# Performance work log

Hardware: AMD Instinct MI355X
Metric: run time of the kernel (lower is better)

The kernel has to match this reference:

```python
import jax, jax.numpy as jnp
import numpy as np

NUM_HEADS = 32
NUM_KV_HEADS = 8
HEAD_DIM = 128
ROPE_THETA = 10000.0
MAX_SEQ_LEN = 2048


def build_rope_cache(seq_len, head_dim, theta=10000.0):
    freq_indices = jnp.arange(0, head_dim, 2, dtype=jnp.float32)
    inv_freq = 1.0 / theta ** (freq_indices / head_dim)
    positions = jnp.arange(seq_len, dtype=jnp.float32)
    angles = jnp.outer(positions, inv_freq)  # (S, D/2)
    cos = jnp.cos(angles)
    sin = jnp.sin(angles)
    return jnp.concatenate([cos, cos], axis=-1), jnp.concatenate([sin, sin], axis=-1)


def apply_rotary_embedding(x, cos, sin):
    # x: (B, S, H, D); cos/sin: (S, D)
    d = x.shape[-1]
    x1, x2 = x[..., : d // 2], x[..., d // 2 :]
    x_rot = jnp.concatenate([-x2, x1], axis=-1)
    return x * cos[None, :, None, :] + x_rot * sin[None, :, None, :]


def setup_inputs() -> dict:
    key = jax.random.key(0)
    k_x, k_q, k_k, k_v, k_o = jax.random.split(key, 5)
    B, S, HID = 2, 2048, NUM_HEADS * HEAD_DIM
    KV = NUM_KV_HEADS * HEAD_DIM
    x = jax.random.normal(k_x, (B, S, HID), dtype=jnp.float32)
    # causal mask, shape (B, 1, S, S)
    causal = jnp.tril(jnp.ones((S, S), dtype=bool))
    mask = jnp.broadcast_to(causal[None, None], (B, 1, S, S))
    sc_in = 1.0 / np.sqrt(HID)
    Wq = jax.random.normal(k_q, (HID, HID), dtype=jnp.float32) * sc_in
    Wk = jax.random.normal(k_k, (HID, KV), dtype=jnp.float32) * sc_in
    Wv = jax.random.normal(k_v, (HID, KV), dtype=jnp.float32) * sc_in
    Wo = jax.random.normal(k_o, (HID, HID), dtype=jnp.float32) * sc_in
    return {"x": x, "mask": mask, "Wq": Wq, "Wk": Wk, "Wv": Wv, "Wo": Wo}


def reference(x, mask, Wq, Wk, Wv, Wo):
    B, S, _ = x.shape
    q = (x @ Wq).reshape(B, S, NUM_HEADS, HEAD_DIM)
    k = (x @ Wk).reshape(B, S, NUM_KV_HEADS, HEAD_DIM)
    v = (x @ Wv).reshape(B, S, NUM_KV_HEADS, HEAD_DIM)
    cos, sin = build_rope_cache(MAX_SEQ_LEN, HEAD_DIM, ROPE_THETA)
    cos, sin = cos[:S], sin[:S]
    q = apply_rotary_embedding(q, cos, sin)
    k = apply_rotary_embedding(k, cos, sin)
    group = NUM_HEADS // NUM_KV_HEADS
    if group > 1:
        k = jnp.repeat(k, group, axis=2)
        v = jnp.repeat(v, group, axis=2)
    scale = HEAD_DIM ** -0.5
    # (B, H, S, S)
    scores = jnp.einsum("bqhd,bkhd->bhqk", q, k) * scale
    scores = jnp.where(mask, scores, jnp.finfo(jnp.float32).min)
    attn = jax.nn.softmax(scores, axis=-1)
    out = jnp.einsum("bhqk,bkhd->bqhd", attn, v).reshape(B, S, NUM_HEADS * HEAD_DIM)
    return out @ Wo
```

## Files before the change

### kernel.cpp

```cpp
#include <hip/hip_runtime.h>

#define S_LEN   2048
#define HID_DIM 4096
#define NHEADS  32
#define NKVH    8
#define HD      128
#define KV_DIM  1024
#define KV2     2048
#define BS_ROWS 4096

typedef __attribute__((ext_vector_type(4))) float f32x4;
typedef __attribute__((ext_vector_type(8))) short bf16x8;

__device__ __forceinline__ unsigned short f2b(float f) {
  union { float f; unsigned int u; } cv; cv.f = f;
  unsigned int r = (cv.u + 0x7FFFu + ((cv.u >> 16) & 1u)) >> 16;
  return (unsigned short)r;
}
__device__ __forceinline__ float b2f(unsigned short u) {
  union { unsigned int u; float f; } cv; cv.u = ((unsigned int)u) << 16; return cv.f;
}
__device__ __forceinline__ void gload_lds16(const void* g, void* l) {
  __builtin_amdgcn_global_load_lds(
      (const __attribute__((address_space(1))) unsigned int*)g,
      (__attribute__((address_space(3))) unsigned int*)l, 16, 0, 0);
}
__device__ __forceinline__ float exp2fast(float x) {
#if __has_builtin(__builtin_amdgcn_exp2f)
  return __builtin_amdgcn_exp2f(x);
#else
  return exp2f(x);
#endif
}
__device__ __forceinline__ unsigned cvtpk(float a, float b) {
  unsigned r;
  asm("v_cvt_pk_bf16_f32 %0, %1, %2" : "=v"(r) : "v"(a), "v"(b));
  return r;
}
__device__ __forceinline__ void store_out(float* p, float v) { *p = v; }
__device__ __forceinline__ void store_out(unsigned short* p, float v) { *p = f2b(v); }

__global__ void cvt_f32_bf16(const float* __restrict__ in, unsigned short* __restrict__ out, int n4) {
  int i = blockIdx.x * blockDim.x + threadIdx.x;
  if (i >= n4) return;
  f32x4 v = reinterpret_cast<const f32x4*>(in)[i];
  ushort4 o;
  o.x = f2b(v[0]); o.y = f2b(v[1]); o.z = f2b(v[2]); o.w = f2b(v[3]);
  reinterpret_cast<ushort4*>(out)[i] = o;
}

__global__ void transpose_cvt(const float* __restrict__ W, unsigned short* __restrict__ Wt,
                              int K, int N) {
  __shared__ float t[32][33];
  int n0 = blockIdx.x * 32, k0 = blockIdx.y * 32;
  int tx = threadIdx.x, ty = threadIdx.y;
#pragma unroll
  for (int i = 0; i < 4; ++i)
    t[ty + 8 * i][tx] = W[(size_t)(k0 + ty + 8 * i) * N + n0 + tx];
  __syncthreads();
#pragma unroll
  for (int i = 0; i < 4; ++i)
    Wt[(size_t)(n0 + ty + 8 * i) * K + k0 + tx] = f2b(t[tx][ty + 8 * i]);
}

__global__ void transpose_v_k(const unsigned short* __restrict__ KVb, unsigned short* __restrict__ Vt) {
  __shared__ unsigned short t[32][33];
  int c0 = blockIdx.x * 32;
  int r0 = blockIdx.y * 32;
  int tx = threadIdx.x, ty = threadIdx.y;
#pragma unroll
  for (int i = 0; i < 4; ++i)
    t[ty + 8 * i][tx] = KVb[(size_t)(r0 + ty + 8 * i) * KV2 + KV_DIM + c0 + tx];
  __syncthreads();
  int ob = (r0 >> 11) * 1024;
  int oc = r0 & 2047;
#pragma unroll
  for (int i = 0; i < 4; ++i)
    Vt[(size_t)(ob + c0 + ty + 8 * i) * S_LEN + oc + tx] = t[tx][ty + 8 * i];
}

__global__ void rope_table_k(float* __restrict__ cosT, float* __restrict__ sinT) {
  int idx = blockIdx.x * blockDim.x + threadIdx.x;
  if (idx >= S_LEN * 64) return;
  int s = idx >> 6, i = idx & 63;
  float inv = 1.0f / powf(10000.0f, (float)(2 * i) * (1.0f / 128.0f));
  float ang = (float)s * inv;
  cosT[idx] = cosf(ang);
  sinT[idx] = sinf(ang);
}

__global__ void rope_apply_k(unsigned short* __restrict__ X, const float* __restrict__ cosT,
                             const float* __restrict__ sinT, int nheads, int rowstride,
                             float scale, int total) {
  int idx = blockIdx.x * blockDim.x + threadIdx.x;
  if (idx >= total) return;
  int i4 = idx & 15;
  int t = idx >> 4;
  int h = t % nheads;
  int row = t / nheads;
  int s = row & (S_LEN - 1);
  f32x4 c4 = *reinterpret_cast<const f32x4*>(&cosT[(s << 6) + i4 * 4]);
  f32x4 s4 = *reinterpret_cast<const f32x4*>(&sinT[(s << 6) + i4 * 4]);
  size_t base = (size_t)row * rowstride + (size_t)h * HD + i4 * 4;
  ushort4 xa = *reinterpret_cast<const ushort4*>(&X[base]);
  ushort4 xb = *reinterpret_cast<const ushort4*>(&X[base + 64]);
  unsigned short* pa = (unsigned short*)&xa;
  unsigned short* pb = (unsigned short*)&xb;
  ushort4 oa, ob;
  unsigned short* qa = (unsigned short*)&oa;
  unsigned short* qb = (unsigned short*)&ob;
#pragma unroll
  for (int j = 0; j < 4; ++j) {
    float x1 = b2f(pa[j]), x2 = b2f(pb[j]);
    qa[j] = f2b((x1 * c4[j] - x2 * s4[j]) * scale);
    qb[j] = f2b((x2 * c4[j] + x1 * s4[j]) * scale);
  }
  *reinterpret_cast<ushort4*>(&X[base])      = oa;
  *reinterpret_cast<ushort4*>(&X[base + 64]) = ob;
}

template <typename OutT>
__global__ __launch_bounds__(256) void gemm_bt(const unsigned short* __restrict__ A,
                                               const unsigned short* __restrict__ Bt,
                                               OutT* __restrict__ C, int M, int N, int K) {
  __shared__ unsigned short As[128 * 32];
  __shared__ unsigned short Bs[128 * 32];
  const int tid = threadIdx.x;
  const int lane = tid & 63;
  const int wave = tid >> 6;
  int nwg = gridDim.x, wg = blockIdx.x;
  int swz = (nwg % 8 == 0) ? ((wg & 7) * (nwg >> 3) + (wg >> 3)) : wg;
  const int nbn = N >> 7;
  const int bm = swz / nbn, bn = swz % nbn;
  const int m0 = bm << 7, n0 = bn << 7;
  const int wr = wave >> 1, wc = wave & 1;
  const int lr = lane & 15, kb = lane >> 4;

  f32x4 acc[4][4];
#pragma unroll
  for (int i = 0; i < 4; ++i)
#pragma unroll
    for (int j = 0; j < 4; ++j) acc[i][j] = (f32x4){0.f, 0.f, 0.f, 0.f};

  const unsigned short* Ab = A + (size_t)m0 * K;
  const unsigned short* Bb = Bt + (size_t)n0 * K;

  for (int k0 = 0; k0 < K; k0 += 32) {
    __syncthreads();
#pragma unroll
    for (int i = 0; i < 2; ++i) {
      int idx = i * 256 + tid;
      int row = idx >> 2;
      int off = (idx & 3) << 3;
      gload_lds16(Ab + (size_t)row * K + k0 + off, As + row * 32 + off);
      gload_lds16(Bb + (size_t)row * K + k0 + off, Bs + row * 32 + off);
    }
    __syncthreads();

    bf16x8 af[4], bfr[4];
#pragma unroll
    for (int mi = 0; mi < 4; ++mi)
      af[mi] = *reinterpret_cast<const bf16x8*>(As + (wr * 64 + mi * 16 + lr) * 32 + kb * 8);
#pragma unroll
    for (int ni = 0; ni < 4; ++ni)
      bfr[ni] = *reinterpret_cast<const bf16x8*>(Bs + (wc * 64 + ni * 16 + lr) * 32 + kb * 8);
#pragma unroll
    for (int mi = 0; mi < 4; ++mi)
#pragma unroll
      for (int ni = 0; ni < 4; ++ni)
        acc[mi][ni] = __builtin_amdgcn_mfma_f32_16x16x32_bf16(af[mi], bfr[ni], acc[mi][ni], 0, 0, 0);
  }

#pragma unroll
  for (int mi = 0; mi < 4; ++mi)
#pragma unroll
    for (int ni = 0; ni < 4; ++ni)
#pragma unroll
      for (int r = 0; r < 4; ++r) {
        int row = m0 + wr * 64 + mi * 16 + kb * 4 + r;
        int col = n0 + wc * 64 + ni * 16 + lr;
        store_out(&C[(size_t)row * N + col], acc[mi][ni][r]);
      }
}

#define STAGE_HALF(dstBase, Sp, k0, h)                                           \
  {                                                                              \
    _Pragma("unroll")                                                            \
    for (int i_ = 0; i_ < 2; ++i_) {                                             \
      int c_ = i_ * 512 + tid;                                                   \
      int rl_ = c_ >> 3, ch_ = c_ & 7;                                           \
      int row_ = (h) * 128 + rl_;                                                \
      gload_lds16((Sp) + (size_t)row_ * K + (k0) + ((ch_ ^ (row_ & 7)) << 3),    \
                  (char*)(dstBase) + row_ * 128 + ch_ * 16);                     \
    }                                                                            \
  }
#define LDF(buf, R, sw) \
  (*reinterpret_cast<const bf16x8*>((const char*)(buf) + (R) * 128 + (sw)))
#define PHASE_SYNC()                                        \
  __builtin_amdgcn_s_barrier();                             \
  asm volatile("s_waitcnt lgkmcnt(0)" ::: "memory");        \
  __builtin_amdgcn_sched_barrier(0);

template <typename OutT>
__global__ __launch_bounds__(512, 1) void gemm256(const unsigned short* __restrict__ A,
                                                  const unsigned short* __restrict__ Bt,
                                                  OutT* __restrict__ C, int M, int N, int K) {
  __shared__ unsigned short Asl[2][256 * 64];
  __shared__ unsigned short Bsl[2][256 * 64];
  const int tid = threadIdx.x;
  const int lane = tid & 63;
  const int wave = tid >> 6;
  const int wr = wave >> 2;
  const int wc = wave & 3;
  const int lr = lane & 15, kb = lane >> 4;

// ... 71 lines not shown
      for (int ni = 0; ni < 4; ++ni)
        acc[mi][ni] = __builtin_amdgcn_mfma_f32_16x16x32_bf16(af[mi], bfr[ni], acc[mi][ni], 0, 0, 0);
    __builtin_amdgcn_s_setprio(0);
    __builtin_amdgcn_s_barrier();

#pragma unroll
    for (int mi = 0; mi < 4; ++mi) af[mi] = LDF(Acur, wr * 128 + (mi + 4) * 16 + lr, sw1);
    PHASE_SYNC();
    __builtin_amdgcn_s_setprio(1);
#pragma unroll
    for (int mi = 0; mi < 4; ++mi)
#pragma unroll
      for (int ni = 0; ni < 4; ++ni)
        acc[mi + 4][ni] = __builtin_amdgcn_mfma_f32_16x16x32_bf16(af[mi], bfr[ni], acc[mi + 4][ni], 0, 0, 0);
    __builtin_amdgcn_s_setprio(0);
    __builtin_amdgcn_s_barrier();

    if (pf) asm volatile("s_waitcnt vmcnt(0)" ::: "memory");
    __builtin_amdgcn_s_barrier();
  }

#pragma unroll
  for (int mi = 0; mi < 8; ++mi)
#pragma unroll
    for (int ni = 0; ni < 4; ++ni)
#pragma unroll
      for (int r = 0; r < 4; ++r) {
        int row = m0 + wr * 128 + mi * 16 + kb * 4 + r;
        int col = n0 + wc * 64 + ni * 16 + lr;
        store_out(&C[(size_t)row * N + col], acc[mi][ni][r]);
      }
}

__global__ __launch_bounds__(256, 2) void attn_fwd(const unsigned short* __restrict__ Q,
                                                   const unsigned short* __restrict__ KV,
                                                   const unsigned short* __restrict__ Vt,
                                                   const float* __restrict__ cosT,
                                                   const float* __restrict__ sinT,
                                                   unsigned short* __restrict__ O) {
  __shared__ unsigned short Ks[2][64 * 128];
  __shared__ unsigned short Ps[4][2][16 * 72];
  const int tid = threadIdx.x, lane = tid & 63, wave = tid >> 6;
  const int lr = lane & 15, kb = lane >> 4;
  const int pr = blockIdx.x;
  const int bh = blockIdx.y;
  const int b = bh >> 5, h = bh & 31, kvh = h >> 2;
  const unsigned short* Qp = Q + (size_t)b * S_LEN * HID_DIM + (size_t)h * HD;
  const unsigned short* Kp = KV + (size_t)b * S_LEN * KV2 + (size_t)kvh * HD;
  const unsigned short* Vtp = Vt + (size_t)(b * 8 + kvh) * HD * S_LEN;
  unsigned short* Op = O + (size_t)b * S_LEN * HID_DIM + (size_t)h * HD;

#pragma unroll 1
  for (int pass = 0; pass < 2; ++pass) {
    const int qt = pass ? pr : 15 - pr;
    const int q0 = qt * 128;
    int qrowQ[2];
    qrowQ[0] = q0 + wave * 32 + lr;
    qrowQ[1] = q0 + wave * 32 + 16 + lr;

    bf16x8 qf[2][4];
#pragma unroll
    for (int qs = 0; qs < 2; ++qs) {
      const int qrow = qrowQ[qs];
      bf16x8 raw[4];
#pragma unroll
      for (int dc = 0; dc < 4; ++dc)
        raw[dc] = *reinterpret_cast<const bf16x8*>(Qp + (size_t)qrow * HID_DIM + dc * 32 + kb * 8);
      const float* ct = cosT + (qrow << 6) + kb * 8;
      const float* st = sinT + (qrow << 6) + kb * 8;
      f32x4 cv0 = *(const f32x4*)(ct),      cv1 = *(const f32x4*)(ct + 4);
      f32x4 cv2 = *(const f32x4*)(ct + 32), cv3 = *(const f32x4*)(ct + 36);
      f32x4 sv0 = *(const f32x4*)(st),      sv1 = *(const f32x4*)(st + 4);
      f32x4 sv2 = *(const f32x4*)(st + 32), sv3 = *(const f32x4*)(st + 36);
      const float sc = 0.08838834764831843f * 1.4426950408889634f;
#pragma unroll
      for (int j = 0; j < 8; ++j) {
        const int jj = j & 3;
        float c0 = (j < 4) ? cv0[jj] : cv1[jj];
        float s0 = (j < 4) ? sv0[jj] : sv1[jj];
        float c1 = (j < 4) ? cv2[jj] : cv3[jj];
        float s1 = (j < 4) ? sv2[jj] : sv3[jj];
        float a1 = b2f((unsigned short)raw[0][j]), a2 = b2f((unsigned short)raw[2][j]);
        qf[qs][0][j] = (short)f2b((a1 * c0 - a2 * s0) * sc);
        qf[qs][2][j] = (short)f2b((a2 * c0 + a1 * s0) * sc);
        float b1 = b2f((unsigned short)raw[1][j]), b2x = b2f((unsigned short)raw[3][j]);
        qf[qs][1][j] = (short)f2b((b1 * c1 - b2x * s1) * sc);
        qf[qs][3][j] = (short)f2b((b2x * c1 + b1 * s1) * sc);
      }
    }

    f32x4 of[2][8];
#pragma unroll
    for (int qs = 0; qs < 2; ++qs)
#pragma unroll
      for (int i = 0; i < 8; ++i) of[qs][i] = (f32x4){0.f, 0.f, 0.f, 0.f};
    float mrow[2] = {-3.0e38f, -3.0e38f};
    float lrow[2] = {0.f, 0.f};

    const int nsteps = 2 * qt + 2;

#pragma unroll
    for (int i = 0; i < 4; ++i) {
      int c = i * 256 + tid;
      int key = c >> 4;
      int ch = (c & 15) ^ (key & 7);
      gload_lds16(Kp + (size_t)key * KV2 + ch * 8, &Ks[0][0] + c * 8);
    }
    __syncthreads();

#pragma unroll 1
    for (int t = 0; t < nsteps; ++t) {
      const int kv0 = t << 6;
      const unsigned short* Kcur = &Ks[t & 1][0];

      bf16x8 vf[8];
#pragma unroll
      for (int dc2 = 0; dc2 < 8; ++dc2)
        vf[dc2] = *reinterpret_cast<const bf16x8*>(
            Vtp + (size_t)(dc2 * 16 + lr) * S_LEN + kv0 + kb * 8);

      if (t + 1 < nsteps) {
        unsigned short* Knxt = &Ks[(t + 1) & 1][0];
#pragma unroll
        for (int i = 0; i < 4; ++i) {
          int c = i * 256 + tid;
          int key = c >> 4;
          int ch = (c & 15) ^ (key & 7);
          gload_lds16(Kp + (size_t)(kv0 + 64 + key) * KV2 + ch * 8, Knxt + c * 8);
        }
      }

      f32x4 sf[2][4];
#pragma unroll
      for (int qs = 0; qs < 2; ++qs)
#pragma unroll
        for (int ki = 0; ki < 4; ++ki) sf[qs][ki] = (f32x4){0.f, 0.f, 0.f, 0.f};
#pragma unroll
      for (int ki = 0; ki < 4; ++ki)
#pragma unroll
        for (int dc = 0; dc < 4; ++dc) {
          bf16x8 kf = *reinterpret_cast<const bf16x8*>(
              Kcur + (ki * 16 + lr) * 128 + (((dc * 4 + kb) ^ (lr & 7)) << 3));
          sf[0][ki] = __builtin_amdgcn_mfma_f32_16x16x32_bf16(kf, qf[0][dc], sf[0][ki], 0, 0, 0);
          sf[1][ki] = __builtin_amdgcn_mfma_f32_16x16x32_bf16(kf, qf[1][dc], sf[1][ki], 0, 0, 0);
        }

#pragma unroll
      for (int qs = 0; qs < 2; ++qs) {
        if (kv0 + 63 > q0 + wave * 32 + qs * 16) {
          const int thr = qrowQ[qs] - kv0;
#pragma unroll
          for (int ki = 0; ki < 4; ++ki)
#pragma unroll
            for (int r = 0; r < 4; ++r)
              if (ki * 16 + kb * 4 + r > thr) sf[qs][ki][r] = -3.0e38f;
        }
      }

#pragma unroll
      for (int qs = 0; qs < 2; ++qs) {
        float m8 = -3.0e38f;
#pragma unroll
        for (int ki = 0; ki < 4; ++ki)
#pragma unroll
          for (int r = 0; r < 4; ++r) m8 = fmaxf(m8, sf[qs][ki][r]);
        m8 = fmaxf(m8, __shfl_xor(m8, 16));
        m8 = fmaxf(m8, __shfl_xor(m8, 32));
        if (__any(m8 > mrow[qs] + 11.5f)) {
          float mn = fmaxf(mrow[qs], m8);
          float corr = exp2fast(mrow[qs] - mn);
          lrow[qs] *= corr;
#pragma unroll
          for (int r = 0; r < 4; ++r) {
            float cr = __shfl(corr, kb * 4 + r);
#pragma unroll
            for (int dc2 = 0; dc2 < 8; ++dc2) of[qs][dc2][r] *= cr;
          }
          mrow[qs] = mn;
        }
        float rs = 0.f;
#pragma unroll
        for (int ki = 0; ki < 4; ++ki) {
          float p0 = exp2fast(sf[qs][ki][0] - mrow[qs]);
          float p1 = exp2fast(sf[qs][ki][1] - mrow[qs]);
          float p2 = exp2fast(sf[qs][ki][2] - mrow[qs]);
          float p3 = exp2fast(sf[qs][ki][3] - mrow[qs]);
          rs += (p0 + p1) + (p2 + p3);
          uint2 w;
          w.x = cvtpk(p0, p1);
          w.y = cvtpk(p2, p3);
          *reinterpret_cast<uint2*>(&Ps[wave][qs][lr * 72 + ki * 16 + kb * 4]) = w;
        }
        rs += __shfl_xor(rs, 16);
        rs += __shfl_xor(rs, 32);
        lrow[qs] += rs;
      }
      asm volatile("s_waitcnt lgkmcnt(0)" ::: "memory");
      __builtin_amdgcn_sched_barrier(0);

      {
        bf16x8 pf0 = *reinterpret_cast<const bf16x8*>(&Ps[wave][0][lr * 72 + kb * 8]);
        bf16x8 pf1 = *reinterpret_cast<const bf16x8*>(&Ps[wave][1][lr * 72 + kb * 8]);
#pragma unroll
        for (int dc2 = 0; dc2 < 8; ++dc2) {
          of[0][dc2] = __builtin_amdgcn_mfma_f32_16x16x32_bf16(pf0, vf[dc2], of[0][dc2], 0, 0, 0);
          of[1][dc2] = __builtin_amdgcn_mfma_f32_16x16x32_bf16(pf1, vf[dc2], of[1][dc2], 0, 0, 0);
        }
      }
#pragma unroll
      for (int dc2 = 0; dc2 < 8; ++dc2)
        vf[dc2] = *reinterpret_cast<const bf16x8*>(
            Vtp + (size_t)(dc2 * 16 + lr) * S_LEN + kv0 + 32 + kb * 8);
      {
        bf16x8 pf0 = *reinterpret_cast<const bf16x8*>(&Ps[wave][0][lr * 72 + 32 + kb * 8]);
        bf16x8 pf1 = *reinterpret_cast<const bf16x8*>(&Ps[wave][1][lr * 72 + 32 + kb * 8]);
#pragma unroll
        for (int dc2 = 0; dc2 < 8; ++dc2) {
          of[0][dc2] = __builtin_amdgcn_mfma_f32_16x16x32_bf16(pf0, vf[dc2], of[0][dc2], 0, 0, 0);
          of[1][dc2] = __builtin_amdgcn_mfma_f32_16x16x32_bf16(pf1, vf[dc2], of[1][dc2], 0, 0, 0);
        }
      }

      __syncthreads();
    }

#pragma unroll
    for (int qs = 0; qs < 2; ++qs) {
      float linv[4];
#pragma unroll
      for (int r = 0; r < 4; ++r) linv[r] = 1.0f / __shfl(lrow[qs], kb * 4 + r);
#pragma unroll
      for (int dc2 = 0; dc2 < 8; ++dc2)
#pragma unroll
        for (int r = 0; r < 4; ++r) {
          int qg = q0 + wave * 32 + qs * 16 + kb * 4 + r;
          Op[(size_t)qg * HID_DIM + dc2 * 16 + lr] = f2b(of[qs][dc2][r] * linv[r]);
        }
    }
  }
}

extern "C" void kernel_launch(void* const* d_in, const int* in_sizes, int n_in,
                              void* d_out, int out_size, void* d_ws, size_t ws_size,
                              hipStream_t stream) {
  const float* x  = (const float*)d_in[0];
  const float* Wq = (const float*)d_in[2];
  const float* Wk = (const float*)d_in[3];
  const float* Wv = (const float*)d_in[4];
  const float* Wo = (const float*)d_in[5];
  float* out = (float*)d_out;

  char* ws = (char*)d_ws;
  unsigned short* xb  = (unsigned short*)(ws + 0);
  unsigned short* wtb = (unsigned short*)(ws + 33554432);
  unsigned short* wkt = (unsigned short*)(ws + 67108864);
  unsigned short* wvt = (unsigned short*)(ws + 75497472);
  unsigned short* Qb  = (unsigned short*)(ws + 83886080);
  unsigned short* KVb = (unsigned short*)(ws + 117440512);
  float* cosT = (float*)(ws + 134217728);
  float* sinT = (float*)(ws + 134742016);
  unsigned short* AO  = xb;
  unsigned short* Vtb = wkt;

  cvt_f32_bf16<<<16384, 256, 0, stream>>>(x, xb, (BS_ROWS * HID_DIM) / 4);
  transpose_cvt<<<dim3(128, 128), dim3(32, 8), 0, stream>>>(Wq, wtb, HID_DIM, HID_DIM);
  transpose_cvt<<<dim3(32, 128), dim3(32, 8), 0, stream>>>(Wk, wkt, HID_DIM, KV_DIM);
  transpose_cvt<<<dim3(32, 128), dim3(32, 8), 0, stream>>>(Wv, wvt, HID_DIM, KV_DIM);
  rope_table_k<<<512, 256, 0, stream>>>(cosT, sinT);

  gemm256<unsigned short><<<256, 512, 0, stream>>>(xb, wtb, Qb, BS_ROWS, HID_DIM, HID_DIM);
  gemm_bt<unsigned short><<<512, 256, 0, stream>>>(xb, wkt, KVb, BS_ROWS, KV2, HID_DIM);

  transpose_v_k<<<dim3(32, 128), dim3(32, 8), 0, stream>>>(KVb, Vtb);
  transpose_cvt<<<dim3(128, 128), dim3(32, 8), 0, stream>>>(Wo, wtb, HID_DIM, HID_DIM);

  rope_apply_k<<<2048, 256, 0, stream>>>(KVb, cosT, sinT, NKVH, KV2, 1.0f,
                                         BS_ROWS * NKVH * 16);

  attn_fwd<<<dim3(8, 64), 256, 0, stream>>>(Qb, KVb, Vtb, cosT, sinT, AO);

  gemm256<float><<<256, 512, 0, stream>>>(AO, wtb, out, BS_ROWS, HID_DIM, HID_DIM);
}
```

Before: 559.0 us.

## Merge prep/post-KV kernels and skip fully-masked attention tiles per wave

Fuses the x conversion, Wq/Wk/Wv transposes and rope table into one prep launch, and fuses K rope with the V transpose into one launch, cutting launch count and inter-kernel gaps. In attention, each wave now skips the QK, softmax and PV work and the V loads for KV tiles lying wholly beyond its causal rows. Both V halves are loaded up front, and the softmax/PV for the two query subtiles is interleaved. This raises register pressure from the extra V fragments, and the waves in a block now do uneven amounts of work.

```diff
diff --git a/kernel.cpp b/kernel.cpp
--- a/kernel.cpp
+++ b/kernel.cpp
@@ -40,13 +40,57 @@
 __device__ __forceinline__ void store_out(float* p, float v) { *p = v; }
 __device__ __forceinline__ void store_out(unsigned short* p, float v) { *p = f2b(v); }
 
-__global__ void cvt_f32_bf16(const float* __restrict__ in, unsigned short* __restrict__ out, int n4) {
-  int i = blockIdx.x * blockDim.x + threadIdx.x;
-  if (i >= n4) return;
-  f32x4 v = reinterpret_cast<const f32x4*>(in)[i];
-  ushort4 o;
-  o.x = f2b(v[0]); o.y = f2b(v[1]); o.z = f2b(v[2]); o.w = f2b(v[3]);
-  reinterpret_cast<ushort4*>(out)[i] = o;
+__global__ __launch_bounds__(256) void prep_k(const float* __restrict__ x,
+                                              unsigned short* __restrict__ xb,
+                                              const float* __restrict__ Wq,
+                                              unsigned short* __restrict__ wtb,
+                                              const float* __restrict__ Wk,
+                                              unsigned short* __restrict__ wkt,
+                                              const float* __restrict__ Wv,
+                                              unsigned short* __restrict__ wvt,
+                                              float* __restrict__ cosT,
+                                              float* __restrict__ sinT) {
+  __shared__ float t[32][33];
+  int bid = blockIdx.x;
+  const int tid = threadIdx.x;
+  if (bid < 16384) {
+    int i = bid * 256 + tid;
+    f32x4 v = reinterpret_cast<const f32x4*>(x)[i];
+    ushort4 o;
+    o.x = f2b(v[0]); o.y = f2b(v[1]); o.z = f2b(v[2]); o.w = f2b(v[3]);
+    reinterpret_cast<ushort4*>(xb)[i] = o;
+    return;
+  }
+  bid -= 16384;
+  const float* W; unsigned short* Wt; int Kd, Nd, bx, by;
+  if (bid < 16384) { W = Wq; Wt = wtb; Kd = HID_DIM; Nd = HID_DIM; bx = bid & 127; by = bid >> 7; }
+  else {
+    bid -= 16384;
+    if (bid < 4096) { W = Wk; Wt = wkt; Kd = HID_DIM; Nd = KV_DIM; bx = bid & 31; by = bid >> 5; }
+    else {
+      bid -= 4096;
+      if (bid < 4096) { W = Wv; Wt = wvt; Kd = HID_DIM; Nd = KV_DIM; bx = bid & 31; by = bid >> 5; }
+      else {
+        bid -= 4096;
+        int idx = bid * 256 + tid;
+        int s = idx >> 6, i = idx & 63;
+        float inv = 1.0f / powf(10000.0f, (float)(2 * i) * (1.0f / 128.0f));
+        float ang = (float)s * inv;
+        cosT[idx] = cosf(ang);
+        sinT[idx] = sinf(ang);
+        return;
+      }
+    }
+  }
+  const int tx = tid & 31, ty = tid >> 5;
+  const int n0 = bx * 32, k0 = by * 32;
+#pragma unroll
+  for (int i = 0; i < 4; ++i)
+    t[ty + 8 * i][tx] = W[(size_t)(k0 + ty + 8 * i) * Nd + n0 + tx];
+  __syncthreads();
+#pragma unroll
+  for (int i = 0; i < 4; ++i)
+    Wt[(size_t)(n0 + ty + 8 * i) * Kd + k0 + tx] = f2b(t[tx][ty + 8 * i]);
 }
 
 __global__ void transpose_cvt(const float* __restrict__ W, unsigned short* __restrict__ Wt,
@@ -63,60 +107,53 @@
     Wt[(size_t)(n0 + ty + 8 * i) * K + k0 + tx] = f2b(t[tx][ty + 8 * i]);
 }
 
-__global__ void transpose_v_k(const unsigned short* __restrict__ KVb, unsigned short* __restrict__ Vt) {
-  __shared__ unsigned short t[32][33];
-  int c0 = blockIdx.x * 32;
-  int r0 = blockIdx.y * 32;
-  int tx = threadIdx.x, ty = threadIdx.y;
+__global__ __launch_bounds__(256) void postkv_k(unsigned short* __restrict__ KVb,
+                                                unsigned short* __restrict__ Vt,
+                                                const float* __restrict__ cosT,
+                                                const float* __restrict__ sinT) {
+  __shared__ unsigned short tsh[32][33];
+  int bid = blockIdx.x;
+  const int tid = threadIdx.x;
+  if (bid < 2048) {
+    int idx = bid * 256 + tid;
+    int i4 = idx & 15;
+    int t = idx >> 4;
+    int h = t & (NKVH - 1);
+    int row = t >> 3;
+    int s = row & (S_LEN - 1);
+    f32x4 c4 = *reinterpret_cast<const f32x4*>(&cosT[(s << 6) + i4 * 4]);
+    f32x4 s4 = *reinterpret_cast<const f32x4*>(&sinT[(s << 6) + i4 * 4]);
+    size_t base = (size_t)row * KV2 + (size_t)h * HD + i4 * 4;
+    ushort4 xa = *reinterpret_cast<const ushort4*>(&KVb[base]);
+    ushort4 xb2 = *reinterpret_cast<const ushort4*>(&KVb[base + 64]);
+    unsigned short* pa = (unsigned short*)&xa;
+    unsigned short* pb = (unsigned short*)&xb2;
+    ushort4 oa, ob;
+    unsigned short* qa = (unsigned short*)&oa;
+    unsigned short* qb = (unsigned short*)&ob;
+#pragma unroll
+    for (int j = 0; j < 4; ++j) {
+      float x1 = b2f(pa[j]), x2 = b2f(pb[j]);
+      qa[j] = f2b(x1 * c4[j] - x2 * s4[j]);
+      qb[j] = f2b(x2 * c4[j] + x1 * s4[j]);
+    }
+    *reinterpret_cast<ushort4*>(&KVb[base])      = oa;
+    *reinterpret_cast<ushort4*>(&KVb[base + 64]) = ob;
+    return;
+  }
+  bid -= 2048;
+  const int tx = tid & 31, ty = tid >> 5;
+  int c0 = (bid & 31) * 32;
+  int r0 = (bid >> 5) * 32;
 #pragma unroll
   for (int i = 0; i < 4; ++i)
-    t[ty + 8 * i][tx] = KVb[(size_t)(r0 + ty + 8 * i) * KV2 + KV_DIM + c0 + tx];
+    tsh[ty + 8 * i][tx] = KVb[(size_t)(r0 + ty + 8 * i) * KV2 + KV_DIM + c0 + tx];
   __syncthreads();
-  int ob = (r0 >> 11) * 1024;
+  int ob2 = (r0 >> 11) * 1024;
   int oc = r0 & 2047;
 #pragma unroll
   for (int i = 0; i < 4; ++i)
-    Vt[(size_t)(ob + c0 + ty + 8 * i) * S_LEN + oc + tx] = t[tx][ty + 8 * i];
-}
-
-__global__ void rope_table_k(float* __restrict__ cosT, float* __restrict__ sinT) {
-  int idx = blockIdx.x * blockDim.x + threadIdx.x;
-  if (idx >= S_LEN * 64) return;
-  int s = idx >> 6, i = idx & 63;
-  float inv = 1.0f / powf(10000.0f, (float)(2 * i) * (1.0f / 128.0f));
-  float ang = (float)s * inv;
-  cosT[idx] = cosf(ang);
-  sinT[idx] = sinf(ang);
-}
-
-__global__ void rope_apply_k(unsigned short* __restrict__ X, const float* __restrict__ cosT,
-                             const float* __restrict__ sinT, int nheads, int rowstride,
-                             float scale, int total) {
-  int idx = blockIdx.x * blockDim.x + threadIdx.x;
-  if (idx >= total) return;
-  int i4 = idx & 15;
-  int t = idx >> 4;
-  int h = t % nheads;
-  int row = t / nheads;
-  int s = row & (S_LEN - 1);
-  f32x4 c4 = *reinterpret_cast<const f32x4*>(&cosT[(s << 6) + i4 * 4]);
-  f32x4 s4 = *reinterpret_cast<const f32x4*>(&sinT[(s << 6) + i4 * 4]);
-  size_t base = (size_t)row * rowstride + (size_t)h * HD + i4 * 4;
-  ushort4 xa = *reinterpret_cast<const ushort4*>(&X[base]);
-  ushort4 xb = *reinterpret_cast<const ushort4*>(&X[base + 64]);
-  unsigned short* pa = (unsigned short*)&xa;
-  unsigned short* pb = (unsigned short*)&xb;
-  ushort4 oa, ob;
-  unsigned short* qa = (unsigned short*)&oa;
-  unsigned short* qb = (unsigned short*)&ob;
-#pragma unroll
-  for (int j = 0; j < 4; ++j) {
-    float x1 = b2f(pa[j]), x2 = b2f(pb[j]);
-    qa[j] = f2b((x1 * c4[j] - x2 * s4[j]) * scale);
-    qb[j] = f2b((x2 * c4[j] + x1 * s4[j]) * scale);
-  }
-  *reinterpret_cast<ushort4*>(&X[base])      = oa;
-  *reinterpret_cast<ushort4*>(&X[base + 64]) = ob;
+    Vt[(size_t)(ob2 + c0 + ty + 8 * i) * S_LEN + oc + tx] = tsh[tx][ty + 8 * i];
 }
 
 template <typename OutT>
@@ -398,12 +435,17 @@
     for (int t = 0; t < nsteps; ++t) {
       const int kv0 = t << 6;
       const unsigned short* Kcur = &Ks[t & 1][0];
-
-      bf16x8 vf[8];
-#pragma unroll
-      for (int dc2 = 0; dc2 < 8; ++dc2)
-        vf[dc2] = *reinterpret_cast<const bf16x8*>(
-            Vtp + (size_t)(dc2 * 16 + lr) * S_LEN + kv0 + kb * 8);
+      const bool active = (kv0 <= q0 + wave * 32 + 31);
+
+      bf16x8 vf0[8], vf1[8];
+      if (active) {
+#pragma unroll
+        for (int dc2 = 0; dc2 < 8; ++dc2) {
+          const unsigned short* vr = Vtp + (size_t)(dc2 * 16 + lr) * S_LEN + kv0 + kb * 8;
+          vf0[dc2] = *reinterpret_cast<const bf16x8*>(vr);
+          vf1[dc2] = *reinterpret_cast<const bf16x8*>(vr + 32);
+        }
+      }
 
       if (t + 1 < nsteps) {
         unsigned short* Knxt = &Ks[(t + 1) & 1][0];
@@ -416,94 +458,134 @@
         }
       }
 
-      f32x4 sf[2][4];
-#pragma unroll
-      for (int qs = 0; qs < 2; ++qs)
-#pragma unroll
-        for (int ki = 0; ki < 4; ++ki) sf[qs][ki] = (f32x4){0.f, 0.f, 0.f, 0.f};
-#pragma unroll
-      for (int ki = 0; ki < 4; ++ki)
-#pragma unroll
-        for (int dc = 0; dc < 4; ++dc) {
-          bf16x8 kf = *reinterpret_cast<const bf16x8*>(
-              Kcur + (ki * 16 + lr) * 128 + (((dc * 4 + kb) ^ (lr & 7)) << 3));
-          sf[0][ki] = __builtin_amdgcn_mfma_f32_16x16x32_bf16(kf, qf[0][dc], sf[0][ki], 0, 0, 0);
-          sf[1][ki] = __builtin_amdgcn_mfma_f32_16x16x32_bf16(kf, qf[1][dc], sf[1][ki], 0, 0, 0);
-        }
-
-#pragma unroll
-      for (int qs = 0; qs < 2; ++qs) {
-        if (kv0 + 63 > q0 + wave * 32 + qs * 16) {
-          const int thr = qrowQ[qs] - kv0;
+      if (active) {
+        f32x4 sf[2][4];
+#pragma unroll
+        for (int qs = 0; qs < 2; ++qs)
+#pragma unroll
+          for (int ki = 0; ki < 4; ++ki) sf[qs][ki] = (f32x4){0.f, 0.f, 0.f, 0.f};
+#pragma unroll
+        for (int ki = 0; ki < 4; ++ki)
+#pragma unroll
+          for (int dc = 0; dc < 4; ++dc) {
+            bf16x8 kf = *reinterpret_cast<const bf16x8*>(
+                Kcur + (ki * 16 + lr) * 128 + (((dc * 4 + kb) ^ (lr & 7)) << 3));
+            sf[0][ki] = __builtin_amdgcn_mfma_f32_16x16x32_bf16(kf, qf[0][dc], sf[0][ki], 0, 0, 0);
+            sf[1][ki] = __builtin_amdgcn_mfma_f32_16x16x32_bf16(kf, qf[1][dc], sf[1][ki], 0, 0, 0);
+          }
+
+#pragma unroll
+        for (int qs = 0; qs < 2; ++qs) {
+          if (kv0 + 63 > q0 + wave * 32 + qs * 16) {
+            const int thr = qrowQ[qs] - kv0;
+#pragma unroll
+            for (int ki = 0; ki < 4; ++ki)
+#pragma unroll
+              for (int r = 0; r < 4; ++r)
+                if (ki * 16 + kb * 4 + r > thr) sf[qs][ki][r] = -3.0e38f;
+          }
+        }
+
+        {
+          const int qs = 0;
+          float m8 = -3.0e38f;
 #pragma unroll
           for (int ki = 0; ki < 4; ++ki)
 #pragma unroll
-            for (int r = 0; r < 4; ++r)
-              if (ki * 16 + kb * 4 + r > thr) sf[qs][ki][r] = -3.0e38f;
-        }
-      }
-
-#pragma unroll
-      for (int qs = 0; qs < 2; ++qs) {
-        float m8 = -3.0e38f;
-#pragma unroll
-        for (int ki = 0; ki < 4; ++ki)
-#pragma unroll
-          for (int r = 0; r < 4; ++r) m8 = fmaxf(m8, sf[qs][ki][r]);
-        m8 = fmaxf(m8, __shfl_xor(m8, 16));
-        m8 = fmaxf(m8, __shfl_xor(m8, 32));
-        if (__any(m8 > mrow[qs] + 11.5f)) {
-          float mn = fmaxf(mrow[qs], m8);
-          float corr = exp2fast(mrow[qs] - mn);
-          lrow[qs] *= corr;
-#pragma unroll
-          for (int r = 0; r < 4; ++r) {
-            float cr = __shfl(corr, kb * 4 + r);
-#pragma unroll
-            for (int dc2 = 0; dc2 < 8; ++dc2) of[qs][dc2][r] *= cr;
-          }
-          mrow[qs] = mn;
-        }
-        float rs = 0.f;
-#pragma unroll
-        for (int ki = 0; ki < 4; ++ki) {
-          float p0 = exp2fast(sf[qs][ki][0] - mrow[qs]);
-          float p1 = exp2fast(sf[qs][ki][1] - mrow[qs]);
-          float p2 = exp2fast(sf[qs][ki][2] - mrow[qs]);
-          float p3 = exp2fast(sf[qs][ki][3] - mrow[qs]);
-          rs += (p0 + p1) + (p2 + p3);
-          uint2 w;
-          w.x = cvtpk(p0, p1);
-          w.y = cvtpk(p2, p3);
-          *reinterpret_cast<uint2*>(&Ps[wave][qs][lr * 72 + ki * 16 + kb * 4]) = w;
-        }
-        rs += __shfl_xor(rs, 16);
-        rs += __shfl_xor(rs, 32);
-        lrow[qs] += rs;
-      }
-      asm volatile("s_waitcnt lgkmcnt(0)" ::: "memory");
-      __builtin_amdgcn_sched_barrier(0);
-
-      {
-        bf16x8 pf0 = *reinterpret_cast<const bf16x8*>(&Ps[wave][0][lr * 72 + kb * 8]);
-        bf16x8 pf1 = *reinterpret_cast<const bf16x8*>(&Ps[wave][1][lr * 72 + kb * 8]);
-#pragma unroll
-        for (int dc2 = 0; dc2 < 8; ++dc2) {
-          of[0][dc2] = __builtin_amdgcn_mfma_f32_16x16x32_bf16(pf0, vf[dc2], of[0][dc2], 0, 0, 0);
-          of[1][dc2] = __builtin_amdgcn_mfma_f32_16x16x32_bf16(pf1, vf[dc2], of[1][dc2], 0, 0, 0);
-        }
-      }
-#pragma unroll
-      for (int dc2 = 0; dc2 < 8; ++dc2)
-        vf[dc2] = *reinterpret_cast<const bf16x8*>(
-            Vtp + (size_t)(dc2 * 16 + lr) * S_LEN + kv0 + 32 + kb * 8);
-      {
-        bf16x8 pf0 = *reinterpret_cast<const bf16x8*>(&Ps[wave][0][lr * 72 + 32 + kb * 8]);
-        bf16x8 pf1 = *reinterpret_cast<const bf16x8*>(&Ps[wave][1][lr * 72 + 32 + kb * 8]);
-#pragma unroll
-        for (int dc2 = 0; dc2 < 8; ++dc2) {
-          of[0][dc2] = __builtin_amdgcn_mfma_f32_16x16x32_bf16(pf0, vf[dc2], of[0][dc2], 0, 0, 0);
-          of[1][dc2] = __builtin_amdgcn_mfma_f32_16x16x32_bf16(pf1, vf[dc2], of[1][dc2], 0, 0, 0);
+            for (int r = 0; r < 4; ++r) m8 = fmaxf(m8, sf[qs][ki][r]);
+          m8 = fmaxf(m8, __shfl_xor(m8, 16));
+          m8 = fmaxf(m8, __shfl_xor(m8, 32));
+          if (__any(m8 > mrow[qs] + 11.5f)) {
+            float mn = fmaxf(mrow[qs], m8);
+            float corr = exp2fast(mrow[qs] - mn);
+            lrow[qs] *= corr;
+#pragma unroll
+            for (int r = 0; r < 4; ++r) {
+              float cr = __shfl(corr, kb * 4 + r);
+#pragma unroll
+              for (int dc2 = 0; dc2 < 8; ++dc2) of[qs][dc2][r] *= cr;
+            }
+            mrow[qs] = mn;
+          }
+          float rs = 0.f;
+#pragma unroll
+          for (int ki = 0; ki < 4; ++ki) {
+            float p0 = exp2fast(sf[qs][ki][0] - mrow[qs]);
+            float p1 = exp2fast(sf[qs][ki][1] - mrow[qs]);
+            float p2 = exp2fast(sf[qs][ki][2] - mrow[qs]);
+            float p3 = exp2fast(sf[qs][ki][3] - mrow[qs]);
+            rs += (p0 + p1) + (p2 + p3);
+            uint2 w;
+            w.x = cvtpk(p0, p1);
+            w.y = cvtpk(p2, p3);
+            *reinterpret_cast<uint2*>(&Ps[wave][qs][lr * 72 + ki * 16 + kb * 4]) = w;
+          }
+          rs += __shfl_xor(rs, 16);
+          rs += __shfl_xor(rs, 32);
+          lrow[qs] += rs;
+        }
+        asm volatile("s_waitcnt lgkmcnt(0)" ::: "memory");
+        __builtin_amdgcn_sched_barrier(0);
+
+        {
+          bf16x8 pfA = *reinterpret_cast<const bf16x8*>(&Ps[wave][0][lr * 72 + kb * 8]);
+          bf16x8 pfB = *reinterpret_cast<const bf16x8*>(&Ps[wave][0][lr * 72 + 32 + kb * 8]);
+#pragma unroll
+          for (int dc2 = 0; dc2 < 8; ++dc2) {
+            of[0][dc2] = __builtin_amdgcn_mfma_f32_16x16x32_bf16(pfA, vf0[dc2], of[0][dc2], 0, 0, 0);
+            of[0][dc2] = __builtin_amdgcn_mfma_f32_16x16x32_bf16(pfB, vf1[dc2], of[0][dc2], 0, 0, 0);
+          }
+        }
+
+        {
+          const int qs = 1;
+          float m8 = -3.0e38f;
+#pragma unroll
+          for (int ki = 0; ki < 4; ++ki)
+#pragma unroll
+            for (int r = 0; r < 4; ++r) m8 = fmaxf(m8, sf[qs][ki][r]);
+          m8 = fmaxf(m8, __shfl_xor(m8, 16));
+          m8 = fmaxf(m8, __shfl_xor(m8, 32));
+          if (__any(m8 > mrow[qs] + 11.5f)) {
+            float mn = fmaxf(mrow[qs], m8);
+            float corr = exp2fast(mrow[qs] - mn);
+            lrow[qs] *= corr;
+#pragma unroll
+            for (int r = 0; r < 4; ++r) {
+              float cr = __shfl(corr, kb * 4 + r);
+#pragma unroll
+              for (int dc2 = 0; dc2 < 8; ++dc2) of[qs][dc2][r] *= cr;
+            }
+            mrow[qs] = mn;
+          }
+          float rs = 0.f;
+#pragma unroll
+          for (int ki = 0; ki < 4; ++ki) {
+            float p0 = exp2fast(sf[qs][ki][0] - mrow[qs]);
+            float p1 = exp2fast(sf[qs][ki][1] - mrow[qs]);
+            float p2 = exp2fast(sf[qs][ki][2] - mrow[qs]);
+            float p3 = exp2fast(sf[qs][ki][3] - mrow[qs]);
+            rs += (p0 + p1) + (p2 + p3);
+            uint2 w;
+            w.x = cvtpk(p0, p1);
+            w.y = cvtpk(p2, p3);
+            *reinterpret_cast<uint2*>(&Ps[wave][qs][lr * 72 + ki * 16 + kb * 4]) = w;
+          }
+          rs += __shfl_xor(rs, 16);
+          rs += __shfl_xor(rs, 32);
+          lrow[qs] += rs;
+        }
+        asm volatile("s_waitcnt lgkmcnt(0)" ::: "memory");
+        __builtin_amdgcn_sched_barrier(0);
+
+        {
+          bf16x8 pfC = *reinterpret_cast<const bf16x8*>(&Ps[wave][1][lr * 72 + kb * 8]);
+          bf16x8 pfD = *reinterpret_cast<const bf16x8*>(&Ps[wave][1][lr * 72 + 32 + kb * 8]);
+#pragma unroll
+          for (int dc2 = 0; dc2 < 8; ++dc2) {
+            of[1][dc2] = __builtin_amdgcn_mfma_f32_16x16x32_bf16(pfC, vf0[dc2], of[1][dc2], 0, 0, 0);
+            of[1][dc2] = __builtin_amdgcn_mfma_f32_16x16x32_bf16(pfD, vf1[dc2], of[1][dc2], 0, 0, 0);
+          }
         }
       }
 
@@ -548,20 +630,13 @@
   unsigned short* AO  = xb;
   unsigned short* Vtb = wkt;
 
-  cvt_f32_bf16<<<16384, 256, 0, stream>>>(x, xb, (BS_ROWS * HID_DIM) / 4);
-  transpose_cvt<<<dim3(128, 128), dim3(32, 8), 0, stream>>>(Wq, wtb, HID_DIM, HID_DIM);
-  transpose_cvt<<<dim3(32, 128), dim3(32, 8), 0, stream>>>(Wk, wkt, HID_DIM, KV_DIM);
-  transpose_cvt<<<dim3(32, 128), dim3(32, 8), 0, stream>>>(Wv, wvt, HID_DIM, KV_DIM);
-  rope_table_k<<<512, 256, 0, stream>>>(cosT, sinT);
+  prep_k<<<41472, 256, 0, stream>>>(x, xb, Wq, wtb, Wk, wkt, Wv, wvt, cosT, sinT);
 
   gemm256<unsigned short><<<256, 512, 0, stream>>>(xb, wtb, Qb, BS_ROWS, HID_DIM, HID_DIM);
   gemm_bt<unsigned short><<<512, 256, 0, stream>>>(xb, wkt, KVb, BS_ROWS, KV2, HID_DIM);
 
-  transpose_v_k<<<dim3(32, 128), dim3(32, 8), 0, stream>>>(KVb, Vtb);
   transpose_cvt<<<dim3(128, 128), dim3(32, 8), 0, stream>>>(Wo, wtb, HID_DIM, HID_DIM);
-
-  rope_apply_k<<<2048, 256, 0, stream>>>(KVb, cosT, sinT, NKVH, KV2, 1.0f,
-                                         BS_ROWS * NKVH * 16);
+  postkv_k<<<6144, 256, 0, stream>>>(KVb, Vtb, cosT, sinT);
 
   attn_fwd<<<dim3(8, 64), 256, 0, stream>>>(Qb, KVb, Vtb, cosT, sinT, AO);
 
```

New measurement: 554.6 us. Within noise of the previous version (-0.8%).

## Fuse Q/K/V projections into one GEMM and merge prep kernels

Applied to the files above, without the earlier changes.

Concatenates the transposed Wq, Wk and Wv into one weight matrix so a single gemm256 call produces a combined QKV buffer with row stride 6144. This replaces the separate Q GEMM and the smaller-tile K/V GEMM. It also merges the input conversion, weight transposes and rope table into one prep launch, and merges the K rope, V transpose and Wo transpose into one post-GEMM launch. The attention kernel now reads Q and K from the strided combined buffer. The aims are fewer launches, better GEMM tile efficiency and fuller occupancy, at the cost of branchy multi-role kernels and wider strides in the attention reads.

```diff
diff --git a/kernel.cpp b/kernel.cpp
--- a/kernel.cpp
+++ b/kernel.cpp
@@ -6,7 +6,7 @@
 #define NKVH    8
 #define HD      128
 #define KV_DIM  1024
-#define KV2     2048
+#define QKS     6144
 #define BS_ROWS 4096
 
 typedef __attribute__((ext_vector_type(4))) float f32x4;
@@ -40,147 +40,123 @@
 __device__ __forceinline__ void store_out(float* p, float v) { *p = v; }
 __device__ __forceinline__ void store_out(unsigned short* p, float v) { *p = f2b(v); }
 
-__global__ void cvt_f32_bf16(const float* __restrict__ in, unsigned short* __restrict__ out, int n4) {
-  int i = blockIdx.x * blockDim.x + threadIdx.x;
-  if (i >= n4) return;
-  f32x4 v = reinterpret_cast<const f32x4*>(in)[i];
-  ushort4 o;
-  o.x = f2b(v[0]); o.y = f2b(v[1]); o.z = f2b(v[2]); o.w = f2b(v[3]);
-  reinterpret_cast<ushort4*>(out)[i] = o;
-}
-
-__global__ void transpose_cvt(const float* __restrict__ W, unsigned short* __restrict__ Wt,
-                              int K, int N) {
+__global__ __launch_bounds__(256) void prep_k(const float* __restrict__ x,
+                                              unsigned short* __restrict__ xb,
+                                              const float* __restrict__ Wq,
+                                              unsigned short* __restrict__ wtq,
+                                              const float* __restrict__ Wk,
+                                              unsigned short* __restrict__ wtk,
+                                              const float* __restrict__ Wv,
+                                              unsigned short* __restrict__ wtv,
+                                              float* __restrict__ cosT,
+                                              float* __restrict__ sinT) {
   __shared__ float t[32][33];
-  int n0 = blockIdx.x * 32, k0 = blockIdx.y * 32;
-  int tx = threadIdx.x, ty = threadIdx.y;
+  int bid = blockIdx.x;
+  const int tid = threadIdx.x;
+  if (bid < 16384) {
+    int i = bid * 256 + tid;
+    f32x4 v = reinterpret_cast<const f32x4*>(x)[i];
+    ushort4 o;
+    o.x = f2b(v[0]); o.y = f2b(v[1]); o.z = f2b(v[2]); o.w = f2b(v[3]);
+    reinterpret_cast<ushort4*>(xb)[i] = o;
+    return;
+  }
+  bid -= 16384;
+  const float* W; unsigned short* Wt; int Nd, bx, by;
+  if (bid < 16384) { W = Wq; Wt = wtq; Nd = HID_DIM; bx = bid & 127; by = bid >> 7; }
+  else {
+    bid -= 16384;
+    if (bid < 4096) { W = Wk; Wt = wtk; Nd = KV_DIM; bx = bid & 31; by = bid >> 5; }
+    else {
+      bid -= 4096;
+      if (bid < 4096) { W = Wv; Wt = wtv; Nd = KV_DIM; bx = bid & 31; by = bid >> 5; }
+      else {
+        bid -= 4096;
+        int idx = bid * 256 + tid;
+        int s = idx >> 6, i = idx & 63;
+        float inv = 1.0f / powf(10000.0f, (float)(2 * i) * (1.0f / 128.0f));
+        float ang = (float)s * inv;
+        cosT[idx] = cosf(ang);
+        sinT[idx] = sinf(ang);
+        return;
+      }
+    }
+  }
+  const int tx = tid & 31, ty = tid >> 5;
+  const int n0 = bx * 32, k0 = by * 32;
 #pragma unroll
   for (int i = 0; i < 4; ++i)
-    t[ty + 8 * i][tx] = W[(size_t)(k0 + ty + 8 * i) * N + n0 + tx];
+    t[ty + 8 * i][tx] = W[(size_t)(k0 + ty + 8 * i) * Nd + n0 + tx];
   __syncthreads();
 #pragma unroll
   for (int i = 0; i < 4; ++i)
-    Wt[(size_t)(n0 + ty + 8 * i) * K + k0 + tx] = f2b(t[tx][ty + 8 * i]);
-}
-
-__global__ void transpose_v_k(const unsigned short* __restrict__ KVb, unsigned short* __restrict__ Vt) {
-  __shared__ unsigned short t[32][33];
-  int c0 = blockIdx.x * 32;
-  int r0 = blockIdx.y * 32;
-  int tx = threadIdx.x, ty = threadIdx.y;
-#pragma unroll
-  for (int i = 0; i < 4; ++i)
-    t[ty + 8 * i][tx] = KVb[(size_t)(r0 + ty + 8 * i) * KV2 + KV_DIM + c0 + tx];
-  __syncthreads();
-  int ob = (r0 >> 11) * 1024;
-  int oc = r0 & 2047;
-#pragma unroll
-  for (int i = 0; i < 4; ++i)
-    Vt[(size_t)(ob + c0 + ty + 8 * i) * S_LEN + oc + tx] = t[tx][ty + 8 * i];
-}
-
-__global__ void rope_table_k(float* __restrict__ cosT, float* __restrict__ sinT) {
-  int idx = blockIdx.x * blockDim.x + threadIdx.x;
-  if (idx >= S_LEN * 64) return;
-  int s = idx >> 6, i = idx & 63;
-  float inv = 1.0f / powf(10000.0f, (float)(2 * i) * (1.0f / 128.0f));
-  float ang = (float)s * inv;
-  cosT[idx] = cosf(ang);
-  sinT[idx] = sinf(ang);
-}
-
-__global__ void rope_apply_k(unsigned short* __restrict__ X, const float* __restrict__ cosT,
-                             const float* __restrict__ sinT, int nheads, int rowstride,
-                             float scale, int total) {
-  int idx = blockIdx.x * blockDim.x + threadIdx.x;
-  if (idx >= total) return;
-  int i4 = idx & 15;
-  int t = idx >> 4;
-  int h = t % nheads;
-  int row = t / nheads;
-  int s = row & (S_LEN - 1);
-  f32x4 c4 = *reinterpret_cast<const f32x4*>(&cosT[(s << 6) + i4 * 4]);
-  f32x4 s4 = *reinterpret_cast<const f32x4*>(&sinT[(s << 6) + i4 * 4]);
-  size_t base = (size_t)row * rowstride + (size_t)h * HD + i4 * 4;
-  ushort4 xa = *reinterpret_cast<const ushort4*>(&X[base]);
-  ushort4 xb = *reinterpret_cast<const ushort4*>(&X[base + 64]);
-  unsigned short* pa = (unsigned short*)&xa;
-  unsigned short* pb = (unsigned short*)&xb;
-  ushort4 oa, ob;
-  unsigned short* qa = (unsigned short*)&oa;
-  unsigned short* qb = (unsigned short*)&ob;
-#pragma unroll
-  for (int j = 0; j < 4; ++j) {
-    float x1 = b2f(pa[j]), x2 = b2f(pb[j]);
-    qa[j] = f2b((x1 * c4[j] - x2 * s4[j]) * scale);
-    qb[j] = f2b((x2 * c4[j] + x1 * s4[j]) * scale);
-  }
-  *reinterpret_cast<ushort4*>(&X[base])      = oa;
-  *reinterpret_cast<ushort4*>(&X[base + 64]) = ob;
-}
-
-template <typename OutT>
-__global__ __launch_bounds__(256) void gemm_bt(const unsigned short* __restrict__ A,
-                                               const unsigned short* __restrict__ Bt,
-                                               OutT* __restrict__ C, int M, int N, int K) {
-  __shared__ unsigned short As[128 * 32];
-  __shared__ unsigned short Bs[128 * 32];
+    Wt[(size_t)(n0 + ty + 8 * i) * HID_DIM + k0 + tx] = f2b(t[tx][ty + 8 * i]);
+}
+
+__global__ __launch_bounds__(256) void postkv_k(unsigned short* __restrict__ QKVb,
+                                                unsigned short* __restrict__ Vt,
+                                                const float* __restrict__ Wo,
+                                                unsigned short* __restrict__ woT,
+                                                const float* __restrict__ cosT,
+                                                const float* __restrict__ sinT) {
+  __shared__ float tf[32][33];
+  __shared__ unsigned short tsh[32][33];
+  int bid = blockIdx.x;
   const int tid = threadIdx.x;
-  const int lane = tid & 63;
-  const int wave = tid >> 6;
-  int nwg = gridDim.x, wg = blockIdx.x;
-  int swz = (nwg % 8 == 0) ? ((wg & 7) * (nwg >> 3) + (wg >> 3)) : wg;
-  const int nbn = N >> 7;
-  const int bm = swz / nbn, bn = swz % nbn;
-  const int m0 = bm << 7, n0 = bn << 7;
-  const int wr = wave >> 1, wc = wave & 1;
-  const int lr = lane & 15, kb = lane >> 4;
-
-  f32x4 acc[4][4];
-#pragma unroll
-  for (int i = 0; i < 4; ++i)
-#pragma unroll
-    for (int j = 0; j < 4; ++j) acc[i][j] = (f32x4){0.f, 0.f, 0.f, 0.f};
-
-  const unsigned short* Ab = A + (size_t)m0 * K;
-  const unsigned short* Bb = Bt + (size_t)n0 * K;
-
-  for (int k0 = 0; k0 < K; k0 += 32) {
+  if (bid < 2048) {
+    int idx = bid * 256 + tid;
+    int i4 = idx & 15;
+    int t = idx >> 4;
+    int h = t & (NKVH - 1);
+    int row = t >> 3;
+    int s = row & (S_LEN - 1);
+    f32x4 c4 = *reinterpret_cast<const f32x4*>(&cosT[(s << 6) + i4 * 4]);
+    f32x4 s4 = *reinterpret_cast<const f32x4*>(&sinT[(s << 6) + i4 * 4]);
+    size_t base = (size_t)row * QKS + HID_DIM + (size_t)h * HD + i4 * 4;
+    ushort4 xa = *reinterpret_cast<const ushort4*>(&QKVb[base]);
+    ushort4 xb2 = *reinterpret_cast<const ushort4*>(&QKVb[base + 64]);
+    unsigned short* pa = (unsigned short*)&xa;
+    unsigned short* pb = (unsigned short*)&xb2;
+    ushort4 oa, ob;
+    unsigned short* qa = (unsigned short*)&oa;
+    unsigned short* qb = (unsigned short*)&ob;
+#pragma unroll
+    for (int j = 0; j < 4; ++j) {
+      float x1 = b2f(pa[j]), x2 = b2f(pb[j]);
+      qa[j] = f2b(x1 * c4[j] - x2 * s4[j]);
+      qb[j] = f2b(x2 * c4[j] + x1 * s4[j]);
+    }
+    *reinterpret_cast<ushort4*>(&QKVb[base])      = oa;
+    *reinterpret_cast<ushort4*>(&QKVb[base + 64]) = ob;
+    return;
+  }
+  bid -= 2048;
+  const int tx = tid & 31, ty = tid >> 5;
+  if (bid < 4096) {
+    int c0 = (bid & 31) * 32;
+    int r0 = (bid >> 5) * 32;
+#pragma unroll
+    for (int i = 0; i < 4; ++i)
+      tsh[ty + 8 * i][tx] = QKVb[(size_t)(r0 + ty + 8 * i) * QKS + HID_DIM + KV_DIM + c0 + tx];
     __syncthreads();
-#pragma unroll
-    for (int i = 0; i < 2; ++i) {
-      int idx = i * 256 + tid;
-      int row = idx >> 2;
-      int off = (idx & 3) << 3;
-      gload_lds16(Ab + (size_t)row * K + k0 + off, As + row * 32 + off);
-      gload_lds16(Bb + (size_t)row * K + k0 + off, Bs + row * 32 + off);
-    }
+    int ob2 = (r0 >> 11) * 1024;
+    int oc = r0 & 2047;
+#pragma unroll
+    for (int i = 0; i < 4; ++i)
+      Vt[(size_t)(ob2 + c0 + ty + 8 * i) * S_LEN + oc + tx] = tsh[tx][ty + 8 * i];
+    return;
+  }
+  bid -= 4096;
+  {
+    int n0 = (bid & 127) * 32, k0 = (bid >> 7) * 32;
+#pragma unroll
+    for (int i = 0; i < 4; ++i)
+      tf[ty + 8 * i][tx] = Wo[(size_t)(k0 + ty + 8 * i) * HID_DIM + n0 + tx];
     __syncthreads();
-
-    bf16x8 af[4], bfr[4];
-#pragma unroll
-    for (int mi = 0; mi < 4; ++mi)
-      af[mi] = *reinterpret_cast<const bf16x8*>(As + (wr * 64 + mi * 16 + lr) * 32 + kb * 8);
-#pragma unroll
-    for (int ni = 0; ni < 4; ++ni)
-      bfr[ni] = *reinterpret_cast<const bf16x8*>(Bs + (wc * 64 + ni * 16 + lr) * 32 + kb * 8);
-#pragma unroll
-    for (int mi = 0; mi < 4; ++mi)
-#pragma unroll
-      for (int ni = 0; ni < 4; ++ni)
-        acc[mi][ni] = __builtin_amdgcn_mfma_f32_16x16x32_bf16(af[mi], bfr[ni], acc[mi][ni], 0, 0, 0);
-  }
-
-#pragma unroll
-  for (int mi = 0; mi < 4; ++mi)
-#pragma unroll
-    for (int ni = 0; ni < 4; ++ni)
-#pragma unroll
-      for (int r = 0; r < 4; ++r) {
-        int row = m0 + wr * 64 + mi * 16 + kb * 4 + r;
-        int col = n0 + wc * 64 + ni * 16 + lr;
-        store_out(&C[(size_t)row * N + col], acc[mi][ni][r]);
-      }
+#pragma unroll
+    for (int i = 0; i < 4; ++i)
+      woT[(size_t)(n0 + ty + 8 * i) * HID_DIM + k0 + tx] = f2b(tf[tx][ty + 8 * i]);
+  }
 }
 
 #define STAGE_HALF(dstBase, Sp, k0, h)                                           \
@@ -318,8 +294,7 @@
       }
 }
 
-__global__ __launch_bounds__(256, 2) void attn_fwd(const unsigned short* __restrict__ Q,
-                                                   const unsigned short* __restrict__ KV,
+__global__ __launch_bounds__(256, 2) void attn_fwd(const unsigned short* __restrict__ QKV,
                                                    const unsigned short* __restrict__ Vt,
                                                    const float* __restrict__ cosT,
                                                    const float* __restrict__ sinT,
@@ -331,8 +306,8 @@
   const int pr = blockIdx.x;
   const int bh = blockIdx.y;
   const int b = bh >> 5, h = bh & 31, kvh = h >> 2;
-  const unsigned short* Qp = Q + (size_t)b * S_LEN * HID_DIM + (size_t)h * HD;
-  const unsigned short* Kp = KV + (size_t)b * S_LEN * KV2 + (size_t)kvh * HD;
+  const unsigned short* Qp = QKV + (size_t)b * S_LEN * QKS + (size_t)h * HD;
+  const unsigned short* Kp = QKV + (size_t)b * S_LEN * QKS + HID_DIM + (size_t)kvh * HD;
   const unsigned short* Vtp = Vt + (size_t)(b * 8 + kvh) * HD * S_LEN;
   unsigned short* Op = O + (size_t)b * S_LEN * HID_DIM + (size_t)h * HD;
 
@@ -351,7 +326,7 @@
       bf16x8 raw[4];
 #pragma unroll
       for (int dc = 0; dc < 4; ++dc)
-        raw[dc] = *reinterpret_cast<const bf16x8*>(Qp + (size_t)qrow * HID_DIM + dc * 32 + kb * 8);
+        raw[dc] = *reinterpret_cast<const bf16x8*>(Qp + (size_t)qrow * QKS + dc * 32 + kb * 8);
       const float* ct = cosT + (qrow << 6) + kb * 8;
       const float* st = sinT + (qrow << 6) + kb * 8;
       f32x4 cv0 = *(const f32x4*)(ct),      cv1 = *(const f32x4*)(ct + 4);
@@ -390,7 +365,7 @@
       int c = i * 256 + tid;
       int key = c >> 4;
       int ch = (c & 15) ^ (key & 7);
-      gload_lds16(Kp + (size_t)key * KV2 + ch * 8, &Ks[0][0] + c * 8);
+      gload_lds16(Kp + (size_t)key * QKS + ch * 8, &Ks[0][0] + c * 8);
     }
     __syncthreads();
 
@@ -412,7 +387,7 @@
           int c = i * 256 + tid;
           int key = c >> 4;
           int ch = (c & 15) ^ (key & 7);
-          gload_lds16(Kp + (size_t)(kv0 + 64 + key) * KV2 + ch * 8, Knxt + c * 8);
+          gload_lds16(Kp + (size_t)(kv0 + 64 + key) * QKS + ch * 8, Knxt + c * 8);
         }
       }
 
@@ -537,33 +512,26 @@
   float* out = (float*)d_out;
 
   char* ws = (char*)d_ws;
-  unsigned short* xb  = (unsigned short*)(ws + 0);
-  unsigned short* wtb = (unsigned short*)(ws + 33554432);
-  unsigned short* wkt = (unsigned short*)(ws + 67108864);
-  unsigned short* wvt = (unsigned short*)(ws + 75497472);
-  unsigned short* Qb  = (unsigned short*)(ws + 83886080);
-  unsigned short* KVb = (unsigned short*)(ws + 117440512);
+  unsigned short* xb    = (unsigned short*)(ws + 0);
+  unsigned short* wqkvT = (unsigned short*)(ws + 33554432);
+  unsigned short* QKVb  = (unsigned short*)(ws + 83886080);
   float* cosT = (float*)(ws + 134217728);
   float* sinT = (float*)(ws + 134742016);
+  unsigned short* Vtb = wqkvT;
+  unsigned short* woT = (unsigned short*)(ws + 33554432 + 16777216);
   unsigned short* AO  = xb;
-  unsigned short* Vtb = wkt;
-
-  cvt_f32_bf16<<<16384, 256, 0, stream>>>(x, xb, (BS_ROWS * HID_DIM) / 4);
-  transpose_cvt<<<dim3(128, 128), dim3(32, 8), 0, stream>>>(Wq, wtb, HID_DIM, HID_DIM);
-  transpose_cvt<<<dim3(32, 128), dim3(32, 8), 0, stream>>>(Wk, wkt, HID_DIM, KV_DIM);
-  transpose_cvt<<<dim3(32, 128), dim3(32, 8), 0, stream>>>(Wv, wvt, HID_DIM, KV_DIM);
-  rope_table_k<<<512, 256, 0, stream>>>(cosT, sinT);
-
-  gemm256<unsigned short><<<256, 512, 0, stream>>>(xb, wtb, Qb, BS_ROWS, HID_DIM, HID_DIM);
-  gemm_bt<unsigned short><<<512, 256, 0, stream>>>(xb, wkt, KVb, BS_ROWS, KV2, HID_DIM);
-
-  transpose_v_k<<<dim3(32, 128), dim3(32, 8), 0, stream>>>(KVb, Vtb);
-  transpose_cvt<<<dim3(128, 128), dim3(32, 8), 0, stream>>>(Wo, wtb, HID_DIM, HID_DIM);
-
-  rope_apply_k<<<2048, 256, 0, stream>>>(KVb, cosT, sinT, NKVH, KV2, 1.0f,
-                                         BS_ROWS * NKVH * 16);
-
-  attn_fwd<<<dim3(8, 64), 256, 0, stream>>>(Qb, KVb, Vtb, cosT, sinT, AO);
-
-  gemm256<float><<<256, 512, 0, stream>>>(AO, wtb, out, BS_ROWS, HID_DIM, HID_DIM);
-}
+
+  unsigned short* wtq = wqkvT;
+  unsigned short* wtk = wqkvT + (size_t)HID_DIM * HID_DIM;
+  unsigned short* wtv = wtk + (size_t)KV_DIM * HID_DIM;
+
+  prep_k<<<41472, 256, 0, stream>>>(x, xb, Wq, wtq, Wk, wtk, Wv, wtv, cosT, sinT);
+
+  gemm256<unsigned short><<<384, 512, 0, stream>>>(xb, wqkvT, QKVb, BS_ROWS, QKS, HID_DIM);
+
+  postkv_k<<<22528, 256, 0, stream>>>(QKVb, Vtb, Wo, woT, cosT, sinT);
+
+  attn_fwd<<<dim3(8, 64), 256, 0, stream>>>(QKVb, Vtb, cosT, sinT, AO);
+
+  gemm256<float><<<256, 512, 0, stream>>>(AO, woT, out, BS_ROWS, HID_DIM, HID_DIM);
+}
```

New measurement: 547.1 us. 1.02x faster.
